# Performance work log

Measured on AMD Instinct MI355X. Metric: run time of the kernel, lower is better.

## Reference

```python
import jax, jax.numpy as jnp
import numpy as np

N = 50000      # nodes
E = 800000     # edges
T_MAX = 128
N_T = 128
NF = T_MAX * 3 # 384 node features


def setup_inputs() -> dict:
    key = jax.random.key(0)
    ks = jax.random.split(key, 12)
    def lin(k, fi, fo):
        k1, k2 = jax.random.split(k)
        s = 1.0 / np.sqrt(fi)
        return (jax.random.uniform(k1, (fi, fo), jnp.float32, -s, s),
                jax.random.uniform(k2, (fo,), jnp.float32, -s, s))
    x = jax.random.normal(ks[0], (N, NF), jnp.float32)
    edge_index = jax.random.randint(ks[1], (2, E), 0, N, jnp.int32)
    W1, b1 = lin(ks[2], NF, N_T)
    W2, b2 = lin(ks[3], N_T, N_T * 3)
    W3, b3 = lin(ks[4], N_T * 3, N_T * 2)
    W4, b4 = lin(ks[5], N_T * 2, NF)
    Wl, bl = lin(ks[6], NF, T_MAX)
    return {"x": x, "edge_index": edge_index,
            "W1": W1, "b1": b1, "W2": W2, "b2": b2,
            "W3": W3, "b3": b3, "W4": W4, "b4": b4,
            "Wl": Wl, "bl": bl}


def reference(x, edge_index, W1, b1, W2, b2, W3, b3, W4, b4, Wl, bl):
    # GCNConv (PyG defaults): add self-loops, symmetric normalization
    loop = jnp.arange(N, dtype=edge_index.dtype)
    src = jnp.concatenate([edge_index[0], loop])
    dst = jnp.concatenate([edge_index[1], loop])
    deg = jax.ops.segment_sum(jnp.ones_like(src, jnp.float32), dst, num_segments=N)
    dinv = jax.lax.rsqrt(deg)  # deg >= 1 due to self-loops
    norm = (dinv[src] * dinv[dst])[:, None]  # [E+N, 1]

    def gcn(h, W, b):
        hw = h @ W                       # [N, out]
        msg = hw[src] * norm             # gather + scale per edge
        agg = jax.ops.segment_sum(msg, dst, num_segments=N)
        return agg + b

    # dropout is identity in eval mode
    h = jax.nn.leaky_relu(gcn(x, W1, b1))
    h = jax.nn.leaky_relu(gcn(h, W2, b2))
    h = jax.nn.leaky_relu(gcn(h, W3, b3))
    h = jax.nn.leaky_relu(gcn(h, W4, b4))
    h = h @ Wl + bl
    return jax.nn.relu(h)  # args.schedule_deviation == False
```

## Files before the change

### kernel.cpp

```cpp
#include <hip/hip_runtime.h>

#define NNODES 50000
#define NEDGES 800000
#define NTILES ((NNODES + 255) / 256)
#define XFEAT (NNODES * 384)
#define XPREP_BLOCKS (XFEAT / (256 * 8))
#define WPREP_TOTAL 344064
#define WPREP_BLOCKS (WPREP_TOTAL / 256)

typedef unsigned short ushort_t;
typedef __attribute__((ext_vector_type(8))) short short8;
typedef __attribute__((ext_vector_type(4))) float floatx4;

__device__ __forceinline__ float bf2f(unsigned short u) {
  union { unsigned int i; float f; } v; v.i = ((unsigned int)u) << 16; return v.f;
}
__device__ __forceinline__ unsigned short f2bf(float f) {
  union { float f; unsigned int i; } v; v.f = f;
  unsigned int r = v.i + 0x7fffu + ((v.i >> 16) & 1u);
  return (unsigned short)(r >> 16);
}

__device__ __forceinline__ void gload_lds16(const void* g, void* l) {
  __builtin_amdgcn_global_load_lds(
      (const __attribute__((address_space(1))) unsigned int*)g,
      (__attribute__((address_space(3))) unsigned int*)l, 16, 0, 0);
}


__global__ void hist_kernel(const int* dst, int* cnt) {
  int i = blockIdx.x * 256 + threadIdx.x;
  if (i < NEDGES) atomicAdd(&cnt[dst[i]], 1);
}


__global__ __launch_bounds__(256) void tile_scan_kernel(
    const int* __restrict__ cnt, int* __restrict__ tile_pref, int* __restrict__ tile_sum) {
  __shared__ int s[256];
  int b = blockIdx.x, t = threadIdx.x;
  int i = b * 256 + t;
  int v = (i < NNODES) ? cnt[i] : 0;
  s[t] = v;
  __syncthreads();
#pragma unroll
  for (int off = 1; off < 256; off <<= 1) {
    int x = (t >= off) ? s[t - off] : 0;
    __syncthreads();
    s[t] += x;
    __syncthreads();
  }
  if (i < NNODES) tile_pref[i] = s[t] - v;
  if (t == 255) tile_sum[b] = s[255];
}

__global__ __launch_bounds__(256) void sum_scan_kernel(
    const int* __restrict__ tile_sum, int* __restrict__ tile_base) {
  __shared__ int s[256];
  int t = threadIdx.x;
  int v = (t < NTILES) ? tile_sum[t] : 0;
  s[t] = v;
  __syncthreads();
#pragma unroll
  for (int off = 1; off < 256; off <<= 1) {
    int x = (t >= off) ? s[t - off] : 0;
    __syncthreads();
    s[t] += x;
    __syncthreads();
  }
  if (t < NTILES) tile_base[t] = s[t] - v;
}

__global__ __launch_bounds__(256) void scan_write_kernel(
    const int* __restrict__ cnt, const int* __restrict__ tile_pref,
    const int* __restrict__ tile_base, int* __restrict__ row_ptr,
    int* __restrict__ cursor, float* __restrict__ dinv) {
  int b = blockIdx.x, t = threadIdx.x;
  int i = b * 256 + t;
  if (i < NNODES) {
    int base = tile_base[b] + tile_pref[i];
    row_ptr[i] = base;
    cursor[i] = base;
    dinv[i] = rsqrtf((float)(cnt[i] + 1));
    if (i == NNODES - 1) row_ptr[NNODES] = base + cnt[i];
  }
}

__global__ void fill_kernel(const int* src, const int* dst, int* cursor, int* col_idx) {
  int i = blockIdx.x * 256 + threadIdx.x;
  if (i < NEDGES) {
    int p = atomicAdd(&cursor[dst[i]], 1);
    col_idx[p] = src[i];
  }
}

__global__ __launch_bounds__(256) void prep_all(
    const float* __restrict__ x, ushort_t* __restrict__ xbf,
    const float* __restrict__ W1, ushort_t* __restrict__ W1h, ushort_t* __restrict__ W1l,
    const float* __restrict__ W2, ushort_t* __restrict__ W2h, ushort_t* __restrict__ W2l,
    const float* __restrict__ W3, ushort_t* __restrict__ W3h, ushort_t* __restrict__ W3l,
    const float* __restrict__ W4, ushort_t* __restrict__ W4h, ushort_t* __restrict__ W4l,
    const float* __restrict__ Wl, ushort_t* __restrict__ Wlh, ushort_t* __restrict__ Wll) {
  int b = blockIdx.x;
  if (b < XPREP_BLOCKS) {
    size_t i = ((size_t)b * 256 + threadIdx.x) * 8;
    float4 p0 = *(const float4*)(x + i);
    float4 p1 = *(const float4*)(x + i + 4);
    uint4 u;
    u.x = (unsigned int)f2bf(p0.x) | ((unsigned int)f2bf(p0.y) << 16);
    u.y = (unsigned int)f2bf(p0.z) | ((unsigned int)f2bf(p0.w) << 16);
    u.z = (unsigned int)f2bf(p1.x) | ((unsigned int)f2bf(p1.y) << 16);
    u.w = (unsigned int)f2bf(p1.z) | ((unsigned int)f2bf(p1.w) << 16);
    *(uint4*)(xbf + i) = u;
    return;
  }
  int t = (b - XPREP_BLOCKS) * 256 + threadIdx.x;
  const float* W; ushort_t* hi; ushort_t* lo; int K, N;
  if (t < 49152)       { W = W1; hi = W1h; lo = W1l; K = 384; N = 128; }
  else if (t < 98304)  { W = W2; hi = W2h; lo = W2l; K = 128; N = 384; t -= 49152; }
  else if (t < 196608) { W = W3; hi = W3h; lo = W3l; K = 384; N = 256; t -= 98304; }
  else if (t < 294912) { W = W4; hi = W4h; lo = W4l; K = 256; N = 384; t -= 196608; }
  else                 { W = Wl; hi = Wlh; lo = Wll; K = 384; N = 128; t -= 294912; }
  int n = t / K, k = t - n * K;
  float w = W[(size_t)k * N + n];
  unsigned short h = f2bf(w);
  hi[t] = h;
  lo[t] = f2bf(w - bf2f(h));
}


template <int WH>
__device__ __forceinline__ void load_rowh(const ushort_t* p, float* f) {
  if (WH == 1) {
    f[0] = bf2f(*p);
  } else {
    unsigned int u = *(const unsigned int*)p;
    f[0] = bf2f((unsigned short)(u & 0xffff));
    f[1] = bf2f((unsigned short)(u >> 16));
  }
}

template <int C>
__global__ __launch_bounds__(256) void agg_kernel(
    const ushort_t* __restrict__ in, ushort_t* __restrict__ out,
    const int* __restrict__ row_ptr, const int* __restrict__ col_idx,
    const float* __restrict__ dinv, const float* __restrict__ bias,
    int mode, int scale_store) {
  constexpr int WH = C / 128;
  int b = blockIdx.x;
  int half = (b >> 2) & 1;
  int idx = (b >> 3) * 4 + (b & 3);
  if (idx >= 3125) return;
  int wave = idx * 4 + (int)(threadIdx.x >> 6);
  int lane = threadIdx.x & 63;
  int co = half * (C / 2) + lane * WH;
  const ushort_t* base = in + co;
  float bb[WH];
  if (mode) {
    if (WH == 1) {
      bb[0] = bias[co];
    } else {
      float2 b2 = *(const float2*)(bias + co);
      bb[0] = b2.x; bb[1] = b2.y;
    }
  }
  for (int k = 0; k < 4; ++k) {
    int wid = __builtin_amdgcn_readfirstlane(wave * 4 + k);
    float acc[WH];
    load_rowh<WH>(base + (size_t)wid * C, acc);
    int e = row_ptr[wid], e1 = row_ptr[wid + 1];
    for (; e + 16 <= e1; e += 16) {
      int j[16];
#pragma unroll
      for (int q = 0; q < 16; ++q) j[q] = col_idx[e + q];
      float v[16][WH];
#pragma unroll
      for (int q = 0; q < 16; ++q) load_rowh<WH>(base + (size_t)j[q] * C, v[q]);
#pragma unroll
      for (int c = 0; c < WH; ++c) {
        float s0 = (v[0][c] + v[1][c]) + (v[2][c] + v[3][c]);
        float s1 = (v[4][c] + v[5][c]) + (v[6][c] + v[7][c]);
        float s2 = (v[8][c] + v[9][c]) + (v[10][c] + v[11][c]);
        float s3 = (v[12][c] + v[13][c]) + (v[14][c] + v[15][c]);
        acc[c] += (s0 + s1) + (s2 + s3);
      }
    }
    for (; e + 4 <= e1; e += 4) {
      int j0 = col_idx[e], j1 = col_idx[e + 1], j2 = col_idx[e + 2], j3 = col_idx[e + 3];
      float v0[WH], v1[WH], v2[WH], v3[WH];
      load_rowh<WH>(base + (size_t)j0 * C, v0);
      load_rowh<WH>(base + (size_t)j1 * C, v1);
      load_rowh<WH>(base + (size_t)j2 * C, v2);
      load_rowh<WH>(base + (size_t)j3 * C, v3);
#pragma unroll
      for (int c = 0; c < WH; ++c) acc[c] += (v0[c] + v1[c]) + (v2[c] + v3[c]);
    }
    for (; e < e1; ++e) {
      int j = col_idx[e];
      float v[WH];
      load_rowh<WH>(base + (size_t)j * C, v);
#pragma unroll
      for (int c = 0; c < WH; ++c) acc[c] += v[c];
    }
    float di = dinv[wid];
    if (mode) {
      float sc = scale_store ? di : 1.f;
#pragma unroll
      for (int c = 0; c < WH; ++c) {
        float v = acc[c] * di + bb[c];
        v = v > 0.f ? v : 0.01f * v;
        acc[c] = v * sc;
      }
    } else {
#pragma unroll
      for (int c = 0; c < WH; ++c) acc[c] *= di;
    }
    if (WH == 1) {
      out[(size_t)wid * C + co] = f2bf(acc[0]);
    } else {
      *(unsigned int*)(out + (size_t)wid * C + co) =
          (unsigned int)f2bf(acc[0]) | ((unsigned int)f2bf(acc[1]) << 16);
    }
  }
}


#define BK 32

template <int TBM, int TBN>
__global__ __launch_bounds__(256, TBM == 64 ? 6 : 4) void gemm_mfma(
    const ushort_t* __restrict__ A, const ushort_t* __restrict__ Bhi,
    const ushort_t* __restrict__ Blo, void* __restrict__ Cv,
    const float* __restrict__ bias, const float* __restrict__ dinv,
    int M, int K, int ldc, int mode, int scale_store, int out_f32) {
  constexpr int FR = TBM / 32;
  constexpr int FG = TBN / 32;
  constexpr int AIT = TBM / 64;
  constexpr int BIT = TBN / 64;
  __shared__ ushort_t As[TBM * BK];
  __shared__ ushort_t Bh[TBN * BK];
  __shared__ ushort_t Bl[TBN * BK];
  int tid = threadIdx.x;
  int lane = tid & 63, w = tid >> 6;
  int wm = w & 1, wn = w >> 1;
  int m0 = blockIdx.x * TBM, n0 = blockIdx.y * TBN;
  floatx4 acc[FR][FG] = {};
  int nkt = K / BK;
  for (int kt = 0; kt < nkt; ++kt) {
    int kb = kt * BK;
    __syncthreads();
#pragma unroll
    for (int it = 0; it < AIT; ++it) {
      int s = it * 256 + tid;
      int row = s >> 2, ks = (s & 3) * 8;
      int gr = m0 + row; if (gr > M - 1) gr = M - 1;
      gload_lds16(A + (size_t)gr * K + kb + ks,
                  As + (size_t)(it * 256 + w * 64) * 8);
    }
#pragma unroll
    for (int it = 0; it < BIT; ++it) {
      int s = it * 256 + tid;
      int row = s >> 2, ks = (s & 3) * 8;
      gload_lds16(Bhi + (size_t)(n0 + row) * K + kb + ks,
                  Bh + (size_t)(it * 256 + w * 64) * 8);
      gload_lds16(Blo + (size_t)(n0 + row) * K + kb + ks,
                  Bl + (size_t)(it * 256 + w * 64) * 8);
    }
    __syncthreads();
    short8 af[FR], fh[FG], fl[FG];
#pragma unroll
    for (int f = 0; f < FR; ++f)
      af[f] = *(const short8*)&As[(wm * (TBM / 2) + f * 16 + (lane & 15)) * BK + (lane >> 4) * 8];
#pragma unroll
    for (int g = 0; g < FG; ++g) {
      int o = (wn * (TBN / 2) + g * 16 + (lane & 15)) * BK + (lane >> 4) * 8;
      fh[g] = *(const short8*)&Bh[o];
      fl[g] = *(const short8*)&Bl[o];
    }
#pragma unroll
    for (int f = 0; f < FR; ++f)
#pragma unroll
      for (int g = 0; g < FG; ++g) {
        acc[f][g] = __builtin_amdgcn_mfma_f32_16x16x32_bf16(af[f], fh[g], acc[f][g], 0, 0, 0);
        acc[f][g] = __builtin_amdgcn_mfma_f32_16x16x32_bf16(af[f], fl[g], acc[f][g], 0, 0, 0);
      }
  }
  int cr = lane >> 4, cc = lane & 15;
#pragma unroll
  for (int f = 0; f < FR; ++f) {
#pragma unroll
    for (int r = 0; r < 4; ++r) {
      int row = m0 + wm * (TBM / 2) + f * 16 + cr * 4 + r;
      if (row >= M) continue;
      float sc = scale_store ? dinv[row] : 1.f;
#pragma unroll
      for (int g = 0; g < FG; ++g) {
        int col = n0 + wn * (TBN / 2) + g * 16 + cc;
        float v = acc[f][g][r];
        if (mode) {
          v += bias[col];
          v = (mode == 1) ? (v > 0.f ? v : 0.01f * v) : (v > 0.f ? v : 0.f);
        }
        v *= sc;
        if (out_f32) ((float*)Cv)[(size_t)row * ldc + col] = v;
        else ((ushort_t*)Cv)[(size_t)row * ldc + col] = f2bf(v);
      }
    }
  }
}


extern "C" void kernel_launch(void* const* d_in, const int* in_sizes, int n_in,
                              void* d_out, int out_size, void* d_ws, size_t ws_size,
                              hipStream_t stream) {
  const float* x  = (const float*)d_in[0];
  const int* ei   = (const int*)d_in[1];
  const float* W1 = (const float*)d_in[2];
  const float* b1 = (const float*)d_in[3];
  const float* W2 = (const float*)d_in[4];
  const float* b2 = (const float*)d_in[5];
  const float* W3 = (const float*)d_in[6];
  const float* b3 = (const float*)d_in[7];
  const float* W4 = (const float*)d_in[8];
  const float* b4 = (const float*)d_in[9];
  const float* Wl = (const float*)d_in[10];
  const float* bl = (const float*)d_in[11];

  char* p = (char*)d_ws;
  auto alloc = [&](size_t bytes) {
    char* r = p;
    p += (bytes + 255) & ~(size_t)255;
    return r;
  };
  int* cnt       = (int*)alloc((size_t)NNODES * 4);
  int* cursor    = (int*)alloc((size_t)NNODES * 4);
  int* row_ptr   = (int*)alloc((size_t)(NNODES + 1) * 4);
  float* dinv    = (float*)alloc((size_t)NNODES * 4);
  int* col_idx   = (int*)alloc((size_t)NEDGES * 4);
  int* tile_pref = (int*)alloc((size_t)NNODES * 4);
  int* tile_sum  = (int*)alloc(256 * 4);
  int* tile_base = (int*)alloc(256 * 4);
  ushort_t* W1h = (ushort_t*)alloc(49152 * 2); ushort_t* W1l = (ushort_t*)alloc(49152 * 2);
  ushort_t* W2h = (ushort_t*)alloc(49152 * 2); ushort_t* W2l = (ushort_t*)alloc(49152 * 2);
  ushort_t* W3h = (ushort_t*)alloc(98304 * 2); ushort_t* W3l = (ushort_t*)alloc(98304 * 2);
  ushort_t* W4h = (ushort_t*)alloc(98304 * 2); ushort_t* W4l = (ushort_t*)alloc(98304 * 2);
  ushort_t* Wlh = (ushort_t*)alloc(49152 * 2); ushort_t* Wll = (ushort_t*)alloc(49152 * 2);
  ushort_t* actA = (ushort_t*)alloc((size_t)NNODES * 384 * 2);
  ushort_t* actB = (ushort_t*)alloc((size_t)NNODES * 384 * 2);
  ushort_t* xbf = actB;

  const int* src = ei;
  const int* dst = ei + NEDGES;

  hipMemsetAsync(cnt, 0, (size_t)NNODES * 4, stream);
  hist_kernel<<<(NEDGES + 255) / 256, 256, 0, stream>>>(dst, cnt);
  tile_scan_kernel<<<NTILES, 256, 0, stream>>>(cnt, tile_pref, tile_sum);
  sum_scan_kernel<<<1, 256, 0, stream>>>(tile_sum, tile_base);
  scan_write_kernel<<<NTILES, 256, 0, stream>>>(cnt, tile_pref, tile_base, row_ptr, cursor, dinv);
  fill_kernel<<<(NEDGES + 255) / 256, 256, 0, stream>>>(src, dst, cursor, col_idx);

  prep_all<<<XPREP_BLOCKS + WPREP_BLOCKS, 256, 0, stream>>>(
      x, xbf, W1, W1h, W1l, W2, W2h, W2l, W3, W3h, W3l, W4, W4h, W4l, Wl, Wlh, Wll);

  dim3 blk(256);
  int gm64  = (NNODES + 63) / 64;
  int gm128 = (NNODES + 127) / 128;
  int gagg  = 6256;

  gemm_mfma<64, 64><<<dim3(gm64, 2), blk, 0, stream>>>(xbf, W1h, W1l, actA, (const float*)0, dinv, NNODES, 384, 128, 0, 1, 0);
  agg_kernel<128><<<gagg, blk, 0, stream>>>(actA, actB, row_ptr, col_idx, dinv, b1, 1, 1);
  agg_kernel<128><<<gagg, blk, 0, stream>>>(actB, actA, row_ptr, col_idx, dinv, (const float*)0, 0, 0);
  gemm_mfma<128, 128><<<dim3(gm128, 3), blk, 0, stream>>>(actA, W2h, W2l, actB, b2, dinv, NNODES, 128, 384, 1, 0, 0);
  gemm_mfma<128, 128><<<dim3(gm128, 2), blk, 0, stream>>>(actB, W3h, W3l, actA, (const float*)0, dinv, NNODES, 384, 256, 0, 1, 0);
  agg_kernel<256><<<gagg, blk, 0, stream>>>(actA, actB, row_ptr, col_idx, dinv, b3, 1, 1);
  agg_kernel<256><<<gagg, blk, 0, stream>>>(actB, actA, row_ptr, col_idx, dinv, (const float*)0, 0, 0);
  gemm_mfma<128, 128><<<dim3(gm128, 3), blk, 0, stream>>>(actA, W4h, W4l, actB, b4, dinv, NNODES, 256, 384, 1, 0, 0);
  gemm_mfma<64, 64><<<dim3(gm64, 2), blk, 0, stream>>>(actB, Wlh, Wll, d_out, bl, dinv, NNODES, 384, 128, 2, 0, 1);
}
```

Before: 588.0 us.

## Double-buffer GEMM LDS tiles, transpose LDS layout, and remap workgroups across XCDs

The MFMA GEMM now double-buffers its A and B tiles in LDS, issuing global-to-LDS loads for the next K-step before computing on the current one, and drops one barrier per iteration. The LDS layout changes to k-chunk-major (row varies fastest within each 8-element chunk) to cut bank conflicts on fragment reads. Workgroup IDs are remapped so contiguous tiles land on the same XCD for L2 reuse. The cost is doubled LDS use, which lowers the occupancy target for the large-tile variant from 4 to 3.

```diff
diff --git a/kernel.cpp b/kernel.cpp
--- a/kernel.cpp
+++ b/kernel.cpp
@@ -226,55 +226,70 @@
 
 #define BK 32
 
+template <int TB>
+__device__ __forceinline__ void stage_tile(const ushort_t* __restrict__ G, int g0,
+                                           int K, int kb, ushort_t* lds,
+                                           int tid, int w, int Mclamp) {
+  constexpr int IT = TB / 64;
+#pragma unroll
+  for (int it = 0; it < IT; ++it) {
+    int s = it * 256 + tid;
+    int row = s & (TB - 1);
+    int j = s / TB;
+    int gr = g0 + row; if (gr > Mclamp - 1) gr = Mclamp - 1;
+    gload_lds16(G + (size_t)gr * K + kb + j * 8,
+                lds + (size_t)(it * 256 + w * 64) * 8);
+  }
+}
+
 template <int TBM, int TBN>
-__global__ __launch_bounds__(256, TBM == 64 ? 6 : 4) void gemm_mfma(
+__global__ __launch_bounds__(256, TBM == 64 ? 6 : 3) void gemm_mfma(
     const ushort_t* __restrict__ A, const ushort_t* __restrict__ Bhi,
     const ushort_t* __restrict__ Blo, void* __restrict__ Cv,
     const float* __restrict__ bias, const float* __restrict__ dinv,
     int M, int K, int ldc, int mode, int scale_store, int out_f32) {
   constexpr int FR = TBM / 32;
   constexpr int FG = TBN / 32;
-  constexpr int AIT = TBM / 64;
-  constexpr int BIT = TBN / 64;
-  __shared__ ushort_t As[TBM * BK];
-  __shared__ ushort_t Bh[TBN * BK];
-  __shared__ ushort_t Bl[TBN * BK];
+  __shared__ ushort_t As[2][TBM * BK];
+  __shared__ ushort_t Bh[2][TBN * BK];
+  __shared__ ushort_t Bl[2][TBN * BK];
   int tid = threadIdx.x;
   int lane = tid & 63, w = tid >> 6;
   int wm = w & 1, wn = w >> 1;
-  int m0 = blockIdx.x * TBM, n0 = blockIdx.y * TBN;
+
+  int lin = blockIdx.y * gridDim.x + blockIdx.x;
+  int nwg = gridDim.x * gridDim.y;
+  int q = nwg >> 3, r = nwg & 7, xc = lin & 7, sdx = lin >> 3;
+  int wg = (xc < r ? xc * (q + 1) : r * (q + 1) + (xc - r) * q) + sdx;
+  int nty = gridDim.y;
+  int tx = wg / nty, ty = wg - tx * nty;
+  int m0 = tx * TBM, n0 = ty * TBN;
+
   floatx4 acc[FR][FG] = {};
   int nkt = K / BK;
+  int cur = 0;
+  stage_tile<TBM>(A, m0, K, 0, As[0], tid, w, M);
+  stage_tile<TBN>(Bhi, n0, K, 0, Bh[0], tid, w, 1 << 30);
+  stage_tile<TBN>(Blo, n0, K, 0, Bl[0], tid, w, 1 << 30);
+  __syncthreads();
   for (int kt = 0; kt < nkt; ++kt) {
-    int kb = kt * BK;
-    __syncthreads();
-#pragma unroll
-    for (int it = 0; it < AIT; ++it) {
-      int s = it * 256 + tid;
-      int row = s >> 2, ks = (s & 3) * 8;
-      int gr = m0 + row; if (gr > M - 1) gr = M - 1;
-      gload_lds16(A + (size_t)gr * K + kb + ks,
-                  As + (size_t)(it * 256 + w * 64) * 8);
-    }
-#pragma unroll
-    for (int it = 0; it < BIT; ++it) {
-      int s = it * 256 + tid;
-      int row = s >> 2, ks = (s & 3) * 8;
-      gload_lds16(Bhi + (size_t)(n0 + row) * K + kb + ks,
-                  Bh + (size_t)(it * 256 + w * 64) * 8);
-      gload_lds16(Blo + (size_t)(n0 + row) * K + kb + ks,
-                  Bl + (size_t)(it * 256 + w * 64) * 8);
-    }
-    __syncthreads();
+    if (kt + 1 < nkt) {
+      int kb = (kt + 1) * BK;
+      stage_tile<TBM>(A, m0, K, kb, As[cur ^ 1], tid, w, M);
+      stage_tile<TBN>(Bhi, n0, K, kb, Bh[cur ^ 1], tid, w, 1 << 30);
+      stage_tile<TBN>(Blo, n0, K, kb, Bl[cur ^ 1], tid, w, 1 << 30);
+    }
+    __builtin_amdgcn_sched_barrier(0);
     short8 af[FR], fh[FG], fl[FG];
+    int jj = lane >> 4, rr = lane & 15;
 #pragma unroll
     for (int f = 0; f < FR; ++f)
-      af[f] = *(const short8*)&As[(wm * (TBM / 2) + f * 16 + (lane & 15)) * BK + (lane >> 4) * 8];
+      af[f] = *(const short8*)&As[cur][(jj * TBM + wm * (TBM / 2) + f * 16 + rr) * 8];
 #pragma unroll
     for (int g = 0; g < FG; ++g) {
-      int o = (wn * (TBN / 2) + g * 16 + (lane & 15)) * BK + (lane >> 4) * 8;
-      fh[g] = *(const short8*)&Bh[o];
-      fl[g] = *(const short8*)&Bl[o];
+      int o = (jj * TBN + wn * (TBN / 2) + g * 16 + rr) * 8;
+      fh[g] = *(const short8*)&Bh[cur][o];
+      fl[g] = *(const short8*)&Bl[cur][o];
     }
 #pragma unroll
     for (int f = 0; f < FR; ++f)
@@ -283,19 +298,21 @@
         acc[f][g] = __builtin_amdgcn_mfma_f32_16x16x32_bf16(af[f], fh[g], acc[f][g], 0, 0, 0);
         acc[f][g] = __builtin_amdgcn_mfma_f32_16x16x32_bf16(af[f], fl[g], acc[f][g], 0, 0, 0);
       }
+    __syncthreads();
+    cur ^= 1;
   }
   int cr = lane >> 4, cc = lane & 15;
 #pragma unroll
   for (int f = 0; f < FR; ++f) {
 #pragma unroll
-    for (int r = 0; r < 4; ++r) {
-      int row = m0 + wm * (TBM / 2) + f * 16 + cr * 4 + r;
+    for (int r2 = 0; r2 < 4; ++r2) {
+      int row = m0 + wm * (TBM / 2) + f * 16 + cr * 4 + r2;
       if (row >= M) continue;
       float sc = scale_store ? dinv[row] : 1.f;
 #pragma unroll
       for (int g = 0; g < FG; ++g) {
         int col = n0 + wn * (TBN / 2) + g * 16 + cc;
-        float v = acc[f][g][r];
+        float v = acc[f][g][r2];
         if (mode) {
           v += bias[col];
           v = (mode == 1) ? (v > 0.f ? v : 0.01f * v) : (v > 0.f ? v : 0.f);
```

After: 646.2 us. 9.9% more time.
